# Kernel tuning notes

Hardware: AMD Instinct MI355X
Metric: run time of the kernel (lower is better)

Reference implementation:

```python
import jax, jax.numpy as jnp
import numpy as np

IN_SIZE = 3072
HIDDEN = 32
OUT_SIZE = 10
N = 32768


def setup_inputs() -> dict:
    key = jax.random.key(0)
    kx, k1, kb1, k2, kb2 = jax.random.split(key, 5)
    x = jax.random.normal(kx, (N, IN_SIZE), dtype=jnp.float32)
    # torch.nn.Linear default init scale ~ 1/sqrt(fan_in); use scaled normals
    W1 = jax.random.normal(k1, (HIDDEN, IN_SIZE), dtype=jnp.float32) / np.sqrt(IN_SIZE)
    b1 = jax.random.normal(kb1, (HIDDEN,), dtype=jnp.float32) / np.sqrt(IN_SIZE)
    W2 = jax.random.normal(k2, (OUT_SIZE, HIDDEN), dtype=jnp.float32) / np.sqrt(HIDDEN)
    b2 = jax.random.normal(kb2, (OUT_SIZE,), dtype=jnp.float32) / np.sqrt(HIDDEN)
    return {"x": x, "W1": W1, "b1": b1, "W2": W2, "b2": b2}


def reference(x, W1, b1, W2, b2):
    # Batched equivalent of the per-sample loop:
    # y[i] = sigmoid(lin2(relu(lin1(x[i]))))
    h = jax.nn.relu(jnp.einsum('ni,hi->nh', x, W1) + b1)   # (N, 32)
    out = jnp.einsum('nh,oh->no', h, W2) + b2              # (N, out_size)
    return jax.nn.sigmoid(out)
```

## Files before the change

### kernel.cpp

```cpp
#include <hip/hip_runtime.h>
#include <hip/hip_bf16.h>


typedef float  f32x4  __attribute__((ext_vector_type(4)));
typedef short  short8 __attribute__((ext_vector_type(8)));

#define IN_SIZE 3072
#define ROWB    (IN_SIZE * 4)
#define HIDDEN  32
#define OUTS    10
#define NSTAGE  24
#define ABUF_SZ 32768
#define BBUF_SZ 8192

__device__ __forceinline__ unsigned short f2bf(float f) {
    return __builtin_bit_cast(unsigned short, __float2bfloat16(f));
}

__device__ __forceinline__ short8 cvt8(f32x4 a, f32x4 b) {
    short8 r;
    r[0] = (short)f2bf(a[0]); r[1] = (short)f2bf(a[1]);
    r[2] = (short)f2bf(a[2]); r[3] = (short)f2bf(a[3]);
    r[4] = (short)f2bf(b[0]); r[5] = (short)f2bf(b[1]);
    r[6] = (short)f2bf(b[2]); r[7] = (short)f2bf(b[3]);
    return r;
}

__global__ void prep_w1(const float* __restrict__ W1,
                        unsigned short* __restrict__ w1s) {
    int t  = blockIdx.x * 256 + threadIdx.x;
    int l  = t & 63;
    int nt = (t >> 6) & 1;
    int s  = t >> 7;
    int h  = (l & 15) + nt * 16;
    int k  = s * 32 + ((l >> 4) * 8);
    const float* src = W1 + (size_t)h * IN_SIZE + k;
    f32x4 f0 = *(const f32x4*)src;
    f32x4 f1 = *(const f32x4*)(src + 4);
    ((short8*)w1s)[t] = cvt8(f0, f1);
}

typedef __attribute__((address_space(3))) void        lds_void;
typedef const __attribute__((address_space(1))) void  gm_void;

__device__ __forceinline__ void gload16(const void* g, void* l) {
    __builtin_amdgcn_global_load_lds((gm_void*)g, (lds_void*)l, 16, 0, 0);
}

__global__ __launch_bounds__(256, 2)
void mlp_staged(const float* __restrict__ x,
                const float* __restrict__ b1,
                const float* __restrict__ W2,
                const float* __restrict__ b2,
                const unsigned short* __restrict__ w1s,
                float* __restrict__ out) {
    __shared__ __align__(16) unsigned char pool[2 * ABUF_SZ + 2 * BBUF_SZ];

    const int tid = threadIdx.x;
    const int l   = tid & 63;
    const int w   = tid >> 6;
    const int lr  = l & 15;
    const int kg  = l >> 4;
    const int rowbase = blockIdx.x * 64 + w * 16;

    char* ldsA = (char*)pool;
    char* ldsB = (char*)pool + 2 * ABUF_SZ;

    const char* xw   = (const char*)x + (size_t)rowbase * ROWB;
    const char* wsrc = (const char*)w1s;
    const int   rpair = l >> 5;
    const int   pos   = (l & 31) * 16;

    f32x4 acc0 = {0.f, 0.f, 0.f, 0.f};
    f32x4 acc1 = {0.f, 0.f, 0.f, 0.f};

    auto issue = [&](int t) {
        const int buf = t & 1;
        char* da = ldsA + buf * ABUF_SZ + w * 8192;
        const char* xs = xw + (size_t)t * 512 + (size_t)rpair * ROWB + pos;
        #pragma unroll
        for (int j = 0; j < 8; ++j)
            gload16(xs + (size_t)(2 * j) * ROWB, da + j * 1024);
        char* db = ldsB + buf * BBUF_SZ;
        #pragma unroll
        for (int c = 0; c < 2; ++c) {
            const int p = 2 * w + c;
            const char* src = wsrc +
                ((size_t)((t * 4 + (p >> 1)) * 128 + (p & 1) * 64 + l)) * 16;
            gload16(src, db + p * 1024);
        }
    };

    auto compute = [&](int t) {
        const int buf = t & 1;
        const char* A = ldsA + buf * ABUF_SZ + w * 8192 + lr * 512 + kg * 32;
        const char* B = ldsB + buf * BBUF_SZ + l * 16;
        #pragma unroll
        for (int s = 0; s < 4; ++s) {
            f32x4 a0  = *(const f32x4*)(A + s * 128);
            f32x4 a1  = *(const f32x4*)(A + s * 128 + 16);
            short8 bf0 = *(const short8*)(B + (2 * s) * 1024);
            short8 bf1 = *(const short8*)(B + (2 * s + 1) * 1024);
            short8 af = cvt8(a0, a1);
            acc0 = __builtin_amdgcn_mfma_f32_16x16x32_bf16(af, bf0, acc0, 0, 0, 0);
            acc1 = __builtin_amdgcn_mfma_f32_16x16x32_bf16(af, bf1, acc1, 0, 0, 0);
        }
    };

    issue(0);
    #pragma unroll 1
    for (int t = 0; t < NSTAGE; ++t) {
        if (t + 1 < NSTAGE) {
            issue(t + 1);
            asm volatile("s_waitcnt vmcnt(10)" ::: "memory");
        } else {
            asm volatile("s_waitcnt vmcnt(0)" ::: "memory");
        }
        __builtin_amdgcn_s_barrier();
        compute(t);
        asm volatile("" ::: "memory");
        __builtin_amdgcn_s_barrier();
    }

    float* hb = (float*)pool + w * (16 * 36);
    const float bv0 = b1[lr];
    const float bv1 = b1[lr + 16];
    #pragma unroll
    for (int i = 0; i < 4; ++i) {
        float v0 = acc0[i] + bv0; v0 = v0 > 0.f ? v0 : 0.f;
        float v1 = acc1[i] + bv1; v1 = v1 > 0.f ? v1 : 0.f;
        hb[(kg * 4 + i) * 36 + lr]      = v0;
        hb[(kg * 4 + i) * 36 + lr + 16] = v1;
    }
    __syncthreads();

    if (l < 32) {
        const int half = l >> 4;
        const int row  = l & 15;
        f32x4 hv[8];
        const f32x4* hp = (const f32x4*)&hb[row * 36];
        #pragma unroll
        for (int q = 0; q < 8; ++q) hv[q] = hp[q];

        float* op = out + (size_t)(rowbase + row) * OUTS + half * 5;
        #pragma unroll
        for (int oo = 0; oo < 5; ++oo) {
            const int o = half * 5 + oo;
            const f32x4* w2p = (const f32x4*)(W2 + o * HIDDEN);
            f32x4 s4 = {0.f, 0.f, 0.f, 0.f};
            #pragma unroll
            for (int q = 0; q < 8; ++q) s4 += hv[q] * w2p[q];
            float v = b2[o] + s4[0] + s4[1] + s4[2] + s4[3];
            op[oo] = 1.0f / (1.0f + __expf(-v));
        }
    }
}

__global__ __launch_bounds__(256, 2)
void mlp_fallback(const float* __restrict__ x,
                  const float* __restrict__ W1,
                  const float* __restrict__ b1,
                  const float* __restrict__ W2,
                  const float* __restrict__ b2,
                  float* __restrict__ out) {
    __shared__ __align__(16) float hbuf[4][16][36];
    const int tid = threadIdx.x;
    const int l   = tid & 63;
    const int w   = tid >> 6;
    const int lr  = l & 15;
    const int kg  = l >> 4;
    const int rowbase = blockIdx.x * 64 + w * 16;

    const float* xp  = x + (size_t)(rowbase + lr) * IN_SIZE + kg * 8;
    const float* w0p = W1 + (size_t)lr * IN_SIZE + kg * 8;
    const float* w1p = W1 + (size_t)(lr + 16) * IN_SIZE + kg * 8;

    f32x4 acc0 = {0.f, 0.f, 0.f, 0.f};
    f32x4 acc1 = {0.f, 0.f, 0.f, 0.f};
    #pragma unroll 4
    for (int s = 0; s < IN_SIZE / 32; ++s) {
        f32x4 a0 = *(const f32x4*)(xp + s * 32);
        f32x4 a1 = *(const f32x4*)(xp + s * 32 + 4);
        f32x4 c0 = *(const f32x4*)(w0p + s * 32);
        f32x4 c1 = *(const f32x4*)(w0p + s * 32 + 4);
        f32x4 d0 = *(const f32x4*)(w1p + s * 32);
        f32x4 d1 = *(const f32x4*)(w1p + s * 32 + 4);
        short8 af  = cvt8(a0, a1);
        short8 bf0 = cvt8(c0, c1);
        short8 bf1 = cvt8(d0, d1);
        acc0 = __builtin_amdgcn_mfma_f32_16x16x32_bf16(af, bf0, acc0, 0, 0, 0);
        acc1 = __builtin_amdgcn_mfma_f32_16x16x32_bf16(af, bf1, acc1, 0, 0, 0);
    }
    const float bv0 = b1[lr];
    const float bv1 = b1[lr + 16];
    #pragma unroll
    for (int i = 0; i < 4; ++i) {
        float v0 = acc0[i] + bv0; v0 = v0 > 0.f ? v0 : 0.f;
        float v1 = acc1[i] + bv1; v1 = v1 > 0.f ? v1 : 0.f;
        hbuf[w][kg * 4 + i][lr]      = v0;
        hbuf[w][kg * 4 + i][lr + 16] = v1;
    }
    __syncthreads();
    if (l < 32) {
        const int half = l >> 4;
        const int row  = l & 15;
        f32x4 hv[8];
        const f32x4* hp = (const f32x4*)&hbuf[w][row][0];
        #pragma unroll
        for (int q = 0; q < 8; ++q) hv[q] = hp[q];
        float* op = out + (size_t)(rowbase + row) * OUTS + half * 5;
        #pragma unroll
        for (int oo = 0; oo < 5; ++oo) {
            const int o = half * 5 + oo;
            const f32x4* w2p = (const f32x4*)(W2 + o * HIDDEN);
            f32x4 s4 = {0.f, 0.f, 0.f, 0.f};
            #pragma unroll
            for (int q = 0; q < 8; ++q) s4 += hv[q] * w2p[q];
            float v = b2[o] + s4[0] + s4[1] + s4[2] + s4[3];
            op[oo] = 1.0f / (1.0f + __expf(-v));
        }
    }
}

extern "C" void kernel_launch(void* const* d_in, const int* in_sizes, int n_in,
                              void* d_out, int out_size, void* d_ws, size_t ws_size,
                              hipStream_t stream) {
    (void)n_in; (void)out_size;
    const float* x  = (const float*)d_in[0];
    const float* W1 = (const float*)d_in[1];
    const float* b1 = (const float*)d_in[2];
    const float* W2 = (const float*)d_in[3];
    const float* b2 = (const float*)d_in[4];
    float* out = (float*)d_out;

    const int N = in_sizes[0] / IN_SIZE;
    const int nblocks = N / 64;

    const size_t ws_needed = (size_t)(IN_SIZE / 32) * 128 * 16;
    if (ws_size >= ws_needed) {
        unsigned short* w1s = (unsigned short*)d_ws;
        prep_w1<<<dim3(48), dim3(256), 0, stream>>>(W1, w1s);
        mlp_staged<<<dim3(nblocks), dim3(256), 0, stream>>>(
            x, b1, W2, b2, w1s, out);
    } else {
        mlp_fallback<<<dim3(nblocks), dim3(256), 0, stream>>>(
            x, W1, b1, W2, b2, out);
    }
}
```

Baseline: 92.65 us.

## Use 512-thread blocks sharing W1 stage loads and XOR-swizzle x tiles in LDS

The staged kernel now runs 8 waves per block over 128 rows, so each staged W1 slice in LDS serves twice as many rows and each wave issues only one W1 load per stage. The x tile is written to LDS with an XOR swizzle on the 16-byte column, and the compute reads apply the matching swizzle, to reduce LDS bank conflicts on the A-fragment loads. LDS use per block roughly doubles (about 144KB), which limits occupancy to one block per CU, and the wait count is adjusted to the new per-stage load count.

```diff
diff --git a/kernel.cpp b/kernel.cpp
--- a/kernel.cpp
+++ b/kernel.cpp
@@ -10,7 +10,7 @@
 #define HIDDEN  32
 #define OUTS    10
 #define NSTAGE  24
-#define ABUF_SZ 32768
+#define ABUF_SZ 65536
 #define BBUF_SZ 8192
 
 __device__ __forceinline__ unsigned short f2bf(float f) {
@@ -47,7 +47,7 @@
     __builtin_amdgcn_global_load_lds((gm_void*)g, (lds_void*)l, 16, 0, 0);
 }
 
-__global__ __launch_bounds__(256, 2)
+__global__ __launch_bounds__(512, 1)
 void mlp_staged(const float* __restrict__ x,
                 const float* __restrict__ b1,
                 const float* __restrict__ W2,
@@ -61,7 +61,7 @@
     const int w   = tid >> 6;
     const int lr  = l & 15;
     const int kg  = l >> 4;
-    const int rowbase = blockIdx.x * 64 + w * 16;
+    const int rowbase = blockIdx.x * 128 + w * 16;
 
     char* ldsA = (char*)pool;
     char* ldsB = (char*)pool + 2 * ABUF_SZ;
@@ -77,28 +77,29 @@
     auto issue = [&](int t) {
         const int buf = t & 1;
         char* da = ldsA + buf * ABUF_SZ + w * 8192;
-        const char* xs = xw + (size_t)t * 512 + (size_t)rpair * ROWB + pos;
-        #pragma unroll
-        for (int j = 0; j < 8; ++j)
-            gload16(xs + (size_t)(2 * j) * ROWB, da + j * 1024);
-        char* db = ldsB + buf * BBUF_SZ;
-        #pragma unroll
-        for (int c = 0; c < 2; ++c) {
-            const int p = 2 * w + c;
-            const char* src = wsrc +
-                ((size_t)((t * 4 + (p >> 1)) * 128 + (p & 1) * 64 + l)) * 16;
-            gload16(src, db + p * 1024);
-        }
+        #pragma unroll
+        for (int j = 0; j < 8; ++j) {
+            const int row_loc = 2 * j + rpair;
+            const int srcb    = pos ^ ((row_loc & 7) << 4);
+            const char* src = xw + (size_t)row_loc * ROWB + (size_t)t * 512 + srcb;
+            gload16(src, da + j * 1024);
+        }
+        char* db = ldsB + buf * BBUF_SZ + w * 1024;
+        const char* bs = wsrc +
+            ((size_t)((t * 4 + (w >> 1)) * 128 + (w & 1) * 64 + l)) * 16;
+        gload16(bs, db);
     };
 
     auto compute = [&](int t) {
         const int buf = t & 1;
-        const char* A = ldsA + buf * ABUF_SZ + w * 8192 + lr * 512 + kg * 32;
+        const char* A = ldsA + buf * ABUF_SZ + w * 8192 + lr * 512;
         const char* B = ldsB + buf * BBUF_SZ + l * 16;
+        const int swz = (lr & 7) << 4;
         #pragma unroll
         for (int s = 0; s < 4; ++s) {
-            f32x4 a0  = *(const f32x4*)(A + s * 128);
-            f32x4 a1  = *(const f32x4*)(A + s * 128 + 16);
+            const int off = s * 128 + kg * 32;
+            f32x4 a0  = *(const f32x4*)(A + (off ^ swz));
+            f32x4 a1  = *(const f32x4*)(A + ((off + 16) ^ swz));
             short8 bf0 = *(const short8*)(B + (2 * s) * 1024);
             short8 bf1 = *(const short8*)(B + (2 * s + 1) * 1024);
             short8 af = cvt8(a0, a1);
@@ -112,7 +113,7 @@
     for (int t = 0; t < NSTAGE; ++t) {
         if (t + 1 < NSTAGE) {
             issue(t + 1);
-            asm volatile("s_waitcnt vmcnt(10)" ::: "memory");
+            asm volatile("s_waitcnt vmcnt(9)" ::: "memory");
         } else {
             asm volatile("s_waitcnt vmcnt(0)" ::: "memory");
         }
@@ -234,16 +235,15 @@
     float* out = (float*)d_out;
 
     const int N = in_sizes[0] / IN_SIZE;
-    const int nblocks = N / 64;
 
     const size_t ws_needed = (size_t)(IN_SIZE / 32) * 128 * 16;
     if (ws_size >= ws_needed) {
         unsigned short* w1s = (unsigned short*)d_ws;
         prep_w1<<<dim3(48), dim3(256), 0, stream>>>(W1, w1s);
-        mlp_staged<<<dim3(nblocks), dim3(256), 0, stream>>>(
+        mlp_staged<<<dim3(N / 128), dim3(512), 0, stream>>>(
             x, b1, W2, b2, w1s, out);
     } else {
-        mlp_fallback<<<dim3(nblocks), dim3(256), 0, stream>>>(
+        mlp_fallback<<<dim3(N / 64), dim3(256), 0, stream>>>(
             x, W1, b1, W2, b2, out);
     }
 }
```

Result: slower. 96.65 us (+4.3%).
